# Performance work log

Hardware: AMD Instinct MI355X
Metric: run time of the kernel (lower is better)

## Reference

```python
import jax, jax.numpy as jnp
import numpy as np
from jax import lax

H = 8          # num_heads
LAM = 4.0      # lambda_scale
POOL = 8       # pool_ratio (effective, N % POOL == 0)
NS_ITERS = 5
NS_EPS = 1e-4
WHITE_EPS = 1e-5


def _lap_kernel(x, y):
    # x: [B,H,n,D], y: [B,H,m,D] -> exp(-||x_i - y_j||_1 / LAM): [B,H,n,m]
    l1 = jnp.sum(jnp.abs(x[:, :, :, None, :] - y[:, :, None, :, :]), axis=-1)
    return jnp.exp(-l1 / LAM)


def setup_inputs() -> dict:
    key = jax.random.key(0)
    ks = jax.random.split(key, 8)
    B, N, C = 2, 1024, 512
    s = 0.05  # weight scale for realistic magnitudes
    return {
        "x": jax.random.normal(ks[0], (B, N, C), jnp.float32),
        "attention_mask": jnp.ones((B, N), jnp.float32),
        "qkv_w": jax.random.normal(ks[1], (3 * C, C), jnp.float32) * s,
        "qkv_b": jax.random.normal(ks[2], (3 * C,), jnp.float32) * s,
        "proj_w": jax.random.normal(ks[3], (C, C), jnp.float32) * s,
        "proj_b": jax.random.normal(ks[4], (C,), jnp.float32) * s,
        "dwc_w": jax.random.normal(ks[5], (C, 1, 3), jnp.float32) * s,
        "dwc_b": jax.random.normal(ks[6], (C,), jnp.float32) * s,
    }


def reference(x, attention_mask, qkv_w, qkv_b, proj_w, proj_b, dwc_w, dwc_b):
    B, N, C = x.shape
    D = C // H
    tm = attention_mask                      # [B,N]
    mh = tm[:, None, :, None]                # [B,1,N,1] broadcast over heads

    qkv = (x @ qkv_w.T + qkv_b).reshape(B, N, 3, H, D).transpose(2, 0, 3, 1, 4)
    q, k, v = qkv[0] * mh, qkv[1] * mh, qkv[2] * mh   # [B,H,N,D]

    # NOTE: faithful to source: raw reshape of [B,N,H*D] into [B,C,N]
    v_sp = v.transpose(0, 2, 1, 3).reshape(B, C, N)
    q_sp = q.transpose(0, 2, 1, 3).reshape(B, C, N)
    k_sp = k.transpose(0, 2, 1, 3).reshape(B, C, N)

    # depthwise conv1d, kernel 3, padding 1
    v_local = lax.conv_general_dilated(
        v_sp, dwc_w, window_strides=(1,), padding=[(1, 1)],
        feature_group_count=C, dimension_numbers=("NCH", "OIH", "NCH")
    ) + dwc_b[None, :, None]
    v_local = v_local.transpose(0, 2, 1) * tm[:, :, None]   # [B,N,C]

    p = POOL
    m = N // p
    pm = tm.reshape(B, 1, m, p).mean(-1)                    # [B,1,m]
    pms = jnp.clip(pm, 1e-6)
    q_pool = (q_sp * tm[:, None, :]).reshape(B, C, m, p).mean(-1) / pms
    k_pool = (k_sp * tm[:, None, :]).reshape(B, C, m, p).mean(-1) / pms
    lmask = (pm > 0).astype(x.dtype)[:, 0, :]               # [B,m]

    q_l = q_pool.transpose(0, 2, 1).reshape(B, m, H, D).transpose(0, 2, 1, 3)
    k_l = k_pool.transpose(0, 2, 1).reshape(B, m, H, D).transpose(0, 2, 1, 3)

    W = _lap_kernel(q_l, k_l)                               # [B,H,m,m]
    pair = lmask[:, None, :, None] * lmask[:, None, None, :]
    I = jnp.eye(m, dtype=x.dtype)[None, None]
    W = W * pair + I * (1.0 - pair)

    # Newton-Schulz pseudo-inverse
    W_eps = W + NS_EPS * I
    fro = jnp.sqrt(jnp.sum(W_eps * W_eps, axis=(-2, -1), keepdims=True))
    X = (2.0 / (fro + 1e-8)) * jnp.swapaxes(W_eps, -2, -1)
    for _ in range(NS_ITERS):
        X = X @ (2.0 * I - W_eps @ X)
    W_inv = X

    la_mask = lmask[:, None, None, :]                        # [B,1,1,m]
    C_q = _lap_kernel(q, k_l) * la_mask                      # [B,H,N,m]
    C_k = _lap_kernel(k, q_l) * la_mask                      # [B,H,N,m]

    # batch-statistics whitening of C_q over dims (0,2)
    qmask = tm[:, None, :, None]                             # [B,1,N,1]
    valid = jnp.clip(jnp.sum(qmask, axis=(0, 2), keepdims=True), 1.0)
    mu = jnp.sum(C_q * qmask, axis=(0, 2), keepdims=True) / valid
    cen = (C_q - mu) * qmask
    var = jnp.sum(cen * cen, axis=(0, 2), keepdims=True) / valid
    C_q_norm = ((C_q - mu) / jnp.sqrt(var + WHITE_EPS)) * qmask

    context = W_inv @ (jnp.swapaxes(C_k, -2, -1) @ v)        # [B,H,m,D]
    ga = (C_q_norm @ context) * mh                           # [B,H,N,D]
    ga = ga.transpose(0, 2, 1, 3).reshape(B, N, C)

    out = (ga + v_local) @ proj_w.T + proj_b
    return out * tm[:, :, None]
```

## Files before the change

kernel.cpp:

```cpp
#include <hip/hip_runtime.h>
#include <hip/hip_bf16.h>
#include <hip/hip_fp16.h>

#define Hh 8
#define Bz 2
#define Nn 1024
#define Cc 512
#define Dd 64
#define Mm 128
#define NS_EPS 1e-4f
#define WHITE_EPS 1e-5f
#define NEG_L2E_OVER_LAM (-0.3606737602222409f)

__device__ __forceinline__ float h2f(__half v) { return __half2float(v); }
__device__ __forceinline__ __half f2h(float v) { return __float2half(v); }
__device__ __forceinline__ float lapexp(float s) {
  return __builtin_amdgcn_exp2f(s * NEG_L2E_OVER_LAM);
}

typedef _Float16 half8 __attribute__((ext_vector_type(8)));
typedef _Float16 half4v __attribute__((ext_vector_type(4)));
typedef float float4v __attribute__((ext_vector_type(4)));

__global__ __launch_bounds__(256) void qkv_gemm(
    const float* __restrict__ x, const float* __restrict__ w,
    const float* __restrict__ bias, const float* __restrict__ tm,
    __half* __restrict__ Q, __half* __restrict__ K, __half* __restrict__ V) {
  __shared__ _Float16 As[128 * 40];
  __shared__ _Float16 Bs[128 * 40];
  int m0 = blockIdx.x * 128, n0 = blockIdx.y * 128;
  int tid = threadIdx.x;
  int lane = tid & 63, wv = tid >> 6;
  int wm = (wv >> 1) * 64, wn = (wv & 1) * 64;
  int l15 = lane & 15, quad = lane >> 4;
  int srow = tid >> 1, shalf = tid & 1;
  float4v acc[4][4] = {};
  for (int k0 = 0; k0 < 512; k0 += 32) {
    __syncthreads();
    {
      const float4* ga = (const float4*)(x + (size_t)(m0 + srow) * 512 + k0 + shalf * 16);
      const float4* gb = (const float4*)(w + (size_t)(n0 + srow) * 512 + k0 + shalf * 16);
      float4 a0 = ga[0], a1 = ga[1], a2 = ga[2], a3 = ga[3];
      float4 b0 = gb[0], b1 = gb[1], b2 = gb[2], b3 = gb[3];
      half8 ha0 = {(_Float16)a0.x, (_Float16)a0.y, (_Float16)a0.z, (_Float16)a0.w,
                   (_Float16)a1.x, (_Float16)a1.y, (_Float16)a1.z, (_Float16)a1.w};
      half8 ha1 = {(_Float16)a2.x, (_Float16)a2.y, (_Float16)a2.z, (_Float16)a2.w,
                   (_Float16)a3.x, (_Float16)a3.y, (_Float16)a3.z, (_Float16)a3.w};
      half8 hb0 = {(_Float16)b0.x, (_Float16)b0.y, (_Float16)b0.z, (_Float16)b0.w,
                   (_Float16)b1.x, (_Float16)b1.y, (_Float16)b1.z, (_Float16)b1.w};
      half8 hb1 = {(_Float16)b2.x, (_Float16)b2.y, (_Float16)b2.z, (_Float16)b2.w,
                   (_Float16)b3.x, (_Float16)b3.y, (_Float16)b3.z, (_Float16)b3.w};
      int lo = srow * 40 + shalf * 16;
      *(half8*)&As[lo] = ha0;
      *(half8*)&As[lo + 8] = ha1;
      *(half8*)&Bs[lo] = hb0;
      *(half8*)&Bs[lo + 8] = hb1;
    }
    __syncthreads();
    half8 a[4], b[4];
#pragma unroll
    for (int mt = 0; mt < 4; ++mt)
      a[mt] = *(const half8*)&As[(wm + mt * 16 + l15) * 40 + quad * 8];
#pragma unroll
    for (int nt = 0; nt < 4; ++nt)
      b[nt] = *(const half8*)&Bs[(wn + nt * 16 + l15) * 40 + quad * 8];
#pragma unroll
    for (int mt = 0; mt < 4; ++mt)
#pragma unroll
      for (int nt = 0; nt < 4; ++nt)
        acc[mt][nt] =
            __builtin_amdgcn_mfma_f32_16x16x32_f16(a[mt], b[nt], acc[mt][nt], 0, 0, 0);
  }
#pragma unroll
  for (int mt = 0; mt < 4; ++mt) {
#pragma unroll
    for (int r = 0; r < 4; ++r) {
      int row = m0 + wm + mt * 16 + quad * 4 + r;
      int b_ = row >> 10, n_ = row & 1023;
      float t = tm[b_ * 1024 + n_];
#pragma unroll
      for (int nt = 0; nt < 4; ++nt) {
        int c3 = n0 + wn + nt * 16 + l15;
        float v = (acc[mt][nt][r] + bias[c3]) * t;
        int sec = c3 >> 9, ch = c3 & 511;
        __half* dst = (sec == 0) ? Q : (sec == 1 ? K : V);
        dst[(size_t)b_ * (Nn * Cc) + (size_t)n_ * 512 + ch] = f2h(v);
      }
    }
  }
}

__global__ __launch_bounds__(256) void pool_kernel(
    const __half* __restrict__ Q, const __half* __restrict__ K,
    const float* __restrict__ tm, __half* __restrict__ QL,
    __half* __restrict__ KL, float* __restrict__ LM) {
  int ut = blockIdx.x;
  int bh = blockIdx.y;
  int b = bh >> 3, h = bh & 7;
  int u0 = ut * 64;
  int delta = u0 >> 9;
  int ch0 = u0 & 511;
  __shared__ float Qs[64][65];
  __shared__ float Ks[64][65];
  int tid = threadIdx.x;
  for (int e = tid; e < 4096; e += 256) {
    int d = e >> 6, uu = e & 63;
    int row = 2 * (h * 64 + d) + delta;
    size_t gi = (size_t)b * (Nn * Cc) + (size_t)row * 512 + ch0 + uu;
    Qs[d][uu] = h2f(Q[gi]);
    Ks[d][uu] = h2f(K[gi]);
  }
  __syncthreads();
  int d = tid & 63, s = tid >> 6;
#pragma unroll
  for (int jr = 0; jr < 2; ++jr) {
    int jl = s + 4 * jr;
    int j = ut * 8 + jl;
    float pm = 0.f, sq = 0.f, sk = 0.f;
#pragma unroll
    for (int i = 0; i < 8; ++i) {
      float t = tm[b * 1024 + 8 * j + i];
      pm += t;
      sq += Qs[d][8 * jl + i] * t;
      sk += Ks[d][8 * jl + i] * t;
    }
    pm *= 0.125f;
    float pms = fmaxf(pm, 1e-6f);
    size_t oi = ((size_t)bh * 128 + j) * 64 + d;
    QL[oi] = f2h(sq * 0.125f / pms);
    KL[oi] = f2h(sk * 0.125f / pms);
    if (h == 0 && d == 0) LM[b * 128 + j] = (pm > 0.f) ? 1.f : 0.f;
  }
}

__global__ __launch_bounds__(256) void fused_phase1(
    const __half* __restrict__ Q, const __half* __restrict__ K,
    const __half* __restrict__ V, const __half* __restrict__ QL,
    const __half* __restrict__ KL, const float* __restrict__ LM,
    const float* __restrict__ tm, __half* __restrict__ Wh,
    float* __restrict__ KTVp, float* __restrict__ PS,
    __half* __restrict__ Pbuf) {
  __shared__ __align__(16) char smem[31232];
  int id = blockIdx.x;
  int tid = threadIdx.x;
  if (id < 512) {
    int jt = id & 3, bh = (id >> 2) & 15, nc = id >> 6;
    int b = bh >> 3, h = bh & 7;
    int j0 = jt * 32;
    float* kls = (float*)smem;
    float* Qs = (float*)(smem + 8704);
    float* red = (float*)(smem + 17408);
    int sr = tid >> 3, sd8 = (tid & 7) * 8;
    {
      half8 q = *(const half8*)(KL + (size_t)bh * 8192 + (size_t)(j0 + sr) * 64 + sd8);
      float4 f0 = {(float)q[0], (float)q[1], (float)q[2], (float)q[3]};
      float4 f1 = {(float)q[4], (float)q[5], (float)q[6], (float)q[7]};
      *(float4*)&kls[sr * 68 + sd8] = f0;
      *(float4*)&kls[sr * 68 + sd8 + 4] = f1;
    }
    int jq = tid & 15, nq = tid >> 4;
    int jA = j0 + jq * 2, jB = jA + 1;
    float lmA = LM[b * 128 + jA], lmB = LM[b * 128 + jB];
    float aA1 = 0.f, aA2 = 0.f, aA3 = 0.f, aB1 = 0.f, aB2 = 0.f, aB3 = 0.f;
    for (int nt = 0; nt < 4; ++nt) {
      int n0 = nc * 128 + nt * 32;
      __syncthreads();
      {
        size_t gi = (size_t)b * (Nn * Cc) + (size_t)(n0 + sr) * 512 + h * 64 + sd8;
        half8 kv = *(const half8*)(Q + gi);
        float4 k0 = {(float)kv[0], (float)kv[1], (float)kv[2], (float)kv[3]};
        float4 k1 = {(float)kv[4], (float)kv[5], (float)kv[6], (float)kv[7]};
        *(float4*)&Qs[sr * 68 + sd8] = k0;
        *(float4*)&Qs[sr * 68 + sd8 + 4] = k1;
      }
      __syncthreads();
      const float4* q0p = (const float4*)&kls[(jq * 2) * 68];
      const float4* q1p = (const float4*)&kls[(jq * 2 + 1) * 68];
      const float4* k0p = (const float4*)&Qs[(nq * 2) * 68];
      const float4* k1p = (const float4*)&Qs[(nq * 2 + 1) * 68];
      float s00 = 0.f, s01 = 0.f, s10 = 0.f, s11 = 0.f;
#pragma unroll
      for (int i = 0; i < 16; ++i) {
        int dq = (i + tid) & 15;
        float4 q0 = q0p[dq], q1 = q1p[dq];
        float4 k0 = k0p[dq], k1 = k1p[dq];
        s00 += fabsf(q0.x - k0.x) + fabsf(q0.y - k0.y) + fabsf(q0.z - k0.z) + fabsf(q0.w - k0.w);
        s01 += fabsf(q0.x - k1.x) + fabsf(q0.y - k1.y) + fabsf(q0.z - k1.z) + fabsf(q0.w - k1.w);
        s10 += fabsf(q1.x - k0.x) + fabsf(q1.y - k0.y) + fabsf(q1.z - k0.z) + fabsf(q1.w - k0.w);
        s11 += fabsf(q1.x - k1.x) + fabsf(q1.y - k1.y) + fabsf(q1.z - k1.z) + fabsf(q1.w - k1.w);
      }
      int nA = n0 + nq * 2, nB = nA + 1;
      float tA = tm[b * 1024 + nA], tB = tm[b * 1024 + nB];
      float xAa = lapexp(s00) * lmA;
      float xAb = lapexp(s01) * lmA;
      float xBa = lapexp(s10) * lmB;
      float xBb = lapexp(s11) * lmB;
      Pbuf[((size_t)bh * 1024 + nA) * 128 + jA] = f2h(xAa);
      Pbuf[((size_t)bh * 1024 + nB) * 128 + jA] = f2h(xAb);
      Pbuf[((size_t)bh * 1024 + nA) * 128 + jB] = f2h(xBa);
      Pbuf[((size_t)bh * 1024 + nB) * 128 + jB] = f2h(xBb);
      float xt;
      xt = xAa * tA; aA1 += xt; aA2 += xt * xt; aA3 += xt * tA;
      xt = xAb * tB; aA1 += xt; aA2 += xt * xt; aA3 += xt * tB;
      xt = xBa * tA; aB1 += xt; aB2 += xt * xt; aB3 += xt * tA;
      xt = xBb * tB; aB1 += xt; aB2 += xt * xt; aB3 += xt * tB;
    }
    int jl = jq * 2;
    red[(jl * 8 + nq) * 3 + 0] = aA1;
    red[(jl * 8 + nq) * 3 + 1] = aA2;
    red[(jl * 8 + nq) * 3 + 2] = aA3;
    red[((jl + 1) * 8 + nq) * 3 + 0] = aB1;
    red[((jl + 1) * 8 + nq) * 3 + 1] = aB2;
    red[((jl + 1) * 8 + nq) * 3 + 2] = aB3;
    __syncthreads();
    if (tid < 32) {
      float s1 = 0.f, s2 = 0.f, s3 = 0.f;
#pragma unroll
      for (int q = 0; q < 8; ++q) {
        s1 += red[(tid * 8 + q) * 3 + 0];
        s2 += red[(tid * 8 + q) * 3 + 1];
        s3 += red[(tid * 8 + q) * 3 + 2];
      }
      size_t base = ((size_t)(nc * 16 + bh) * 128 + j0 + tid) * 3;
      PS[base] = s1; PS[base + 1] = s2; PS[base + 2] = s3;
    }
  } else if (id < 1024) {
    int kid = id - 512;
    int jt = kid & 7, bh = (kid >> 3) & 15, nc = kid >> 7;
    int b = bh >> 3, h = bh & 7;
    int j0 = jt * 16;
    float* qls = (float*)smem;
    float* Ks = (float*)(smem + 4352);
    float* Vs = (float*)(smem + 13056);
    float* P = (float*)(smem + 21760);
    int sr = tid >> 3, sd8 = (tid & 7) * 8;
    if (tid < 128) {
      half8 q = *(const half8*)(QL + (size_t)bh * 8192 + (size_t)(j0 + sr) * 64 + sd8);
      float4 f0 = {(float)q[0], (float)q[1], (float)q[2], (float)q[3]};
      float4 f1 = {(float)q[4], (float)q[5], (float)q[6], (float)q[7]};
      *(float4*)&qls[sr * 68 + sd8] = f0;
      *(float4*)&qls[sr * 68 + sd8 + 4] = f1;
    }
    int jq = tid & 15, nq = tid >> 4;
    int jl = tid >> 4, dq4 = tid & 15;
    float acc[4] = {};
    for (int nt = 0; nt < 8; ++nt) {
      int n0 = nc * 256 + nt * 32;
      __syncthreads();
      {
        size_t gi = (size_t)b * (Nn * Cc) + (size_t)(n0 + sr) * 512 + h * 64 + sd8;
        half8 kv = *(const half8*)(K + gi);
        half8 vv = *(const half8*)(V + gi);
        float4 k0 = {(float)kv[0], (float)kv[1], (float)kv[2], (float)kv[3]};
        float4 k1 = {(float)kv[4], (float)kv[5], (float)kv[6], (float)kv[7]};
        float4 v0 = {(float)vv[0], (float)vv[1], (float)vv[2], (float)vv[3]};
        float4 v1 = {(float)vv[4], (float)vv[5], (float)vv[6], (float)vv[7]};
        *(float4*)&Ks[sr * 68 + sd8] = k0;
        *(float4*)&Ks[sr * 68 + sd8 + 4] = k1;
        *(float4*)&Vs[sr * 68 + sd8] = v0;
        *(float4*)&Vs[sr * 68 + sd8 + 4] = v1;
      }
      __syncthreads();
      {
        const float4* qp = (const float4*)&qls[jq * 68];
        const float4* k0p = (const float4*)&Ks[(nq * 2) * 68];
        const float4* k1p = (const float4*)&Ks[(nq * 2 + 1) * 68];
        float s0 = 0.f, s1 = 0.f;
#pragma unroll
        for (int i = 0; i < 16; ++i) {
          int dq = (i + tid) & 15;
          float4 qv = qp[dq];
          float4 k0 = k0p[dq], k1 = k1p[dq];
          s0 += fabsf(qv.x - k0.x) + fabsf(qv.y - k0.y) + fabsf(qv.z - k0.z) + fabsf(qv.w - k0.w);
          s1 += fabsf(qv.x - k1.x) + fabsf(qv.y - k1.y) + fabsf(qv.z - k1.z) + fabsf(qv.w - k1.w);
        }
        P[(nq * 2) * 20 + jq] = lapexp(s0);
        P[(nq * 2 + 1) * 20 + jq] = lapexp(s1);
      }
      __syncthreads();
      {
#pragma unroll 8
        for (int n = 0; n < 32; ++n) {
          float p = P[n * 20 + jl];
          float4 v = *(const float4*)&Vs[n * 68 + dq4 * 4];
          acc[0] += p * v.x; acc[1] += p * v.y; acc[2] += p * v.z; acc[3] += p * v.w;
        }
      }
    }
    {
      float lm = LM[b * 128 + j0 + jl];
      float* dst = &KTVp[((size_t)nc * 16 + bh) * 8192 + (size_t)(j0 + jl) * 64 + dq4 * 4];
      float4 o = {acc[0] * lm, acc[1] * lm, acc[2] * lm, acc[3] * lm};
      *(float4*)dst = o;
    }
  } else {
    int wid = id - 1024;
    int it = wid >> 4, bh = wid & 15;
    int b = bh >> 3;
    int i0 = it * 16;
    _Float16* kls16 = (_Float16*)smem;
    float* qs = (float*)(smem + 18432);
    float* ps = (float*)(smem + 22784);
    for (int e = tid; e < 8192; e += 256)
      kls16[(e >> 6) * 72 + (e & 63)] = (_Float16)(*(const _Float16*)&KL[(size_t)bh * 8192 + e]);
    for (int e = tid; e < 1024; e += 256)
      qs[(e >> 6) * 68 + (e & 63)] =
          h2f(QL[(size_t)bh * 8192 + (size_t)(i0 + (e >> 6)) * 64 + (e & 63)]);
    __syncthreads();
    int jg = tid & 63, ng = tid >> 6;
    int j = jg * 2;
    const _Float16* kArow = &kls16[j * 72];
    const _Float16* kBrow = &kls16[(j + 1) * 72];
    float sA[4] = {}, sB[4] = {};
#pragma unroll
    for (int i = 0; i < 16; ++i) {
      int dq = (i + jg) & 15;
      half4v k4a = *(const half4v*)&kArow[dq * 4];
      half4v k4b = *(const half4v*)&kBrow[dq * 4];
      float4 ka = {(float)k4a[0], (float)k4a[1], (float)k4a[2], (float)k4a[3]};
      float4 kb = {(float)k4b[0], (float)k4b[1], (float)k4b[2], (float)k4b[3]};
#pragma unroll
      for (int r = 0; r < 4; ++r) {
        float4 qv = *(const float4*)&qs[(ng * 4 + r) * 68 + dq * 4];
        sA[r] += fabsf(qv.x - ka.x) + fabsf(qv.y - ka.y) + fabsf(qv.z - ka.z) + fabsf(qv.w - ka.w);
        sB[r] += fabsf(qv.x - kb.x) + fabsf(qv.y - kb.y) + fabsf(qv.z - kb.z) + fabsf(qv.w - kb.w);
      }
    }
    float lmA = LM[b * Mm + j], lmB = LM[b * Mm + j + 1];
#pragma unroll
    for (int r = 0; r < 4; ++r) {
      int i = i0 + ng * 4 + r;
      float lmi = LM[b * Mm + i];
      float prA = lmi * lmA, prB = lmi * lmB;
      float dA = (i == j) ? 1.f : 0.f;
      float dB = (i == j + 1) ? 1.f : 0.f;
      ps[(ng * 4 + r) * 132 + j] = lapexp(sA[r]) * prA + dA * (1.f - prA) + dA * NS_EPS;
      ps[(ng * 4 + r) * 132 + j + 1] = lapexp(sB[r]) * prB + dB * (1.f - prB) + dB * NS_EPS;
    }
    __syncthreads();
    for (int e = tid; e < 2048; e += 256)
      Wh[(size_t)bh * (Mm * Mm) + (size_t)(i0 + (e >> 7)) * 128 + (e & 127)] =
          f2h(ps[(e >> 7) * 132 + (e & 127)]);
  }
}

__global__ __launch_bounds__(1024) void fused_phase2(
    const __half* __restrict__ Wh, const float* __restrict__ KTVp,
    const float* __restrict__ PS, const float* __restrict__ tm,
    __half* __restrict__ CTX, float* __restrict__ MU, float* __restrict__ RS) {
  __shared__ __align__(16) char smem[143360];
  int tid = threadIdx.x;
  if (blockIdx.x < 16) {
    int bh = blockIdx.x;
    _Float16* Ws = (_Float16*)smem;
    _Float16* Xa = (_Float16*)(smem + 34816);
    _Float16* Xb = (_Float16*)(smem + 69632);
    _Float16* Tt = (_Float16*)(smem + 104448);
    float* red = (float*)(smem + 139264);
    const __half* Wb = Wh + (size_t)bh * 16384;
    float fro = 0.f;
    for (int e = tid; e < 16384; e += 1024) {
      float wv = h2f(Wb[e]);
      Ws[(e >> 7) * 136 + (e & 127)] = (_Float16)wv;
      fro += wv * wv;
    }
    red[tid] = fro;
    __syncthreads();
    for (int off = 512; off > 0; off >>= 1) {
      if (tid < off) red[tid] += red[tid + off];
      __syncthreads();
    }
    float scale = 2.f / (sqrtf(red[0]) + 1e-8f);
    for (int e = tid; e < 16384; e += 1024) {
      int i = e >> 7, k = e & 127;
      Xa[i * 136 + k] = (_Float16)(scale * (float)Ws[k * 136 + i]);
      Xb[i * 136 + k] = (_Float16)(scale * (float)Ws[i * 136 + k]);
    }
    __syncthreads();
    int lane = tid & 63, wv_ = tid >> 6;
    int wm = (wv_ >> 2) * 32, wn = (wv_ & 3) * 32;
    int l15 = lane & 15, quad = lane >> 4;
    for (int it = 0; it < 5; ++it) {
      {
        float4v acc[2][2] = {};
#pragma unroll
        for (int kt = 0; kt < 4; ++kt) {
          half8 a[2], b[2];
#pragma unroll
          for (int mt = 0; mt < 2; ++mt)
            a[mt] = *(const half8*)&Ws[(wm + mt * 16 + l15) * 136 + kt * 32 + quad * 8];
#pragma unroll
          for (int nt = 0; nt < 2; ++nt)
            b[nt] = *(const half8*)&Xb[(wn + nt * 16 + l15) * 136 + kt * 32 + quad * 8];
#pragma unroll
          for (int mt = 0; mt < 2; ++mt)
#pragma unroll
            for (int nt = 0; nt < 2; ++nt)
              acc[mt][nt] =
                  __builtin_amdgcn_mfma_f32_16x16x32_f16(a[mt], b[nt], acc[mt][nt], 0, 0, 0);
        }
#pragma unroll
        for (int mt = 0; mt < 2; ++mt)
#pragma unroll
          for (int r = 0; r < 4; ++r) {
            int i = wm + mt * 16 + quad * 4 + r;
#pragma unroll
            for (int nt = 0; nt < 2; ++nt) {
              int j = wn + nt * 16 + l15;
              Tt[j * 136 + i] = (_Float16)(((i == j) ? 2.f : 0.f) - acc[mt][nt][r]);
            }
          }
      }
      __syncthreads();
      {
        float4v acc[2][2] = {};
#pragma unroll
        for (int kt = 0; kt < 4; ++kt) {
          half8 a[2], b[2];
#pragma unroll
          for (int mt = 0; mt < 2; ++mt)
            a[mt] = *(const half8*)&Xa[(wm + mt * 16 + l15) * 136 + kt * 32 + quad * 8];
#pragma unroll
          for (int nt = 0; nt < 2; ++nt)
            b[nt] = *(const half8*)&Tt[(wn + nt * 16 + l15) * 136 + kt * 32 + quad * 8];
#pragma unroll
          for (int mt = 0; mt < 2; ++mt)
#pragma unroll
            for (int nt = 0; nt < 2; ++nt)
              acc[mt][nt] =
                  __builtin_amdgcn_mfma_f32_16x16x32_f16(a[mt], b[nt], acc[mt][nt], 0, 0, 0);
        }
        __syncthreads();
#pragma unroll
        for (int mt = 0; mt < 2; ++mt)
#pragma unroll
          for (int r = 0; r < 4; ++r) {
            int i = wm + mt * 16 + quad * 4 + r;
#pragma unroll
            for (int nt = 0; nt < 2; ++nt) {
              int j = wn + nt * 16 + l15;
              _Float16 v = (_Float16)acc[mt][nt][r];
              Xa[i * 136 + j] = v;
              Xb[j * 136 + i] = v;
            }
          }
      }
      __syncthreads();
    }
    float* KTVs = (float*)smem;
    for (int e = tid; e < 8192; e += 1024) {
      float s = KTVp[(size_t)bh * 8192 + e];
#pragma unroll
      for (int nc = 1; nc < 4; ++nc) s += KTVp[((size_t)nc * 16 + bh) * 8192 + e];
      KTVs[(e >> 6) * 68 + (e & 63)] = s;
    }
    __syncthreads();
    int i = tid >> 3, d0 = (tid & 7) * 8;
    float a0 = 0.f, a1 = 0.f, a2 = 0.f, a3 = 0.f;
    float a4 = 0.f, a5 = 0.f, a6 = 0.f, a7 = 0.f;
#pragma unroll 4
    for (int j = 0; j < 128; ++j) {
      float xv = (float)Xa[i * 136 + j];
      float4 k0 = *(const float4*)&KTVs[j * 68 + d0];
      float4 k1 = *(const float4*)&KTVs[j * 68 + d0 + 4];
      a0 += xv * k0.x; a1 += xv * k0.y; a2 += xv * k0.z; a3 += xv * k0.w;
      a4 += xv * k1.x; a5 += xv * k1.y; a6 += xv * k1.z; a7 += xv * k1.w;
    }
    half8 hout = {(_Float16)a0, (_Float16)a1, (_Float16)a2, (_Float16)a3,
                  (_Float16)a4, (_Float16)a5, (_Float16)a6, (_Float16)a7};
    *(half8*)(CTX + (size_t)bh * 8192 + (size_t)i * 64 + d0) = hout;
  } else {
    float (*red2)[2] = (float(*)[2])smem;
    float* ts = (float*)(smem + 8192);
    float a = 0.f, c = 0.f;
    for (int i = tid; i < 2048; i += 1024) { float t = tm[i]; a += t; c += t * t; }
    red2[tid][0] = a; red2[tid][1] = c;
    __syncthreads();
    for (int off = 512; off > 0; off >>= 1) {
      if (tid < off) { red2[tid][0] += red2[tid + off][0]; red2[tid][1] += red2[tid + off][1]; }
      __syncthreads();
    }
    if (tid == 0) { ts[0] = red2[0][0]; ts[1] = red2[0][1]; }
    __syncthreads();
    int hj = tid;
    int h = hj >> 7, j = hj & 127;
    float s1 = 0.f, s2 = 0.f, s3 = 0.f;
#pragma unroll
    for (int nc = 0; nc < 8; ++nc)
#pragma unroll
      for (int b = 0; b < 2; ++b) {
        const float* p = PS + ((size_t)(nc * 16 + b * 8 + h) * 128 + j) * 3;
        s1 += p[0]; s2 += p[1]; s3 += p[2];
      }
    float valid = fmaxf(ts[0], 1.f);
    float mu = s1 / valid;
    float var = (s2 - 2.f * mu * s3 + mu * mu * ts[1]) / valid;
    var = fmaxf(var, 0.f);
    MU[hj] = mu;
    RS[hj] = rsqrtf(var + WHITE_EPS);
  }
}

__global__ __launch_bounds__(256) void ga_fused(
    const __half* __restrict__ Pbuf, const float* __restrict__ MU,
    const float* __restrict__ RS, const __half* __restrict__ CTXg,
    const __half* __restrict__ V, const float* __restrict__ dwc_w,
    const float* __restrict__ dwc_b, const float* __restrict__ tm,
    __half* __restrict__ VL) {
  int bh = blockIdx.y;
  int b = bh >> 3, h = bh & 7;
  int n0 = blockIdx.x * 32;
  __shared__ __half Ps[32][130];
  __shared__ __align__(16) __half2 ctx2[128][32];
  __shared__ float musr[128][2];
  int tid = threadIdx.x;
  for (int e = tid; e < 4096; e += 256)
    Ps[e >> 7][e & 127] = Pbuf[((size_t)bh * 1024 + n0 + (e >> 7)) * 128 + (e & 127)];
  {
    const __half2* cg = (const __half2*)(CTXg + (size_t)bh * 8192);
    for (int e = tid; e < 4096; e += 256) ctx2[e >> 5][e & 31] = cg[e];
  }
  if (tid < 128) { musr[tid][0] = MU[h * 128 + tid]; musr[tid][1] = RS[h * 128 + tid]; }
  __syncthreads();
  int nn = tid >> 4, dq = tid & 15;
  float acc[2][4] = {};
#pragma unroll 2
  for (int j = 0; j < 128; ++j) {
    float mu = musr[j][0], rs = musr[j][1];
    uint2 cc = *(const uint2*)&ctx2[j][dq * 2];
    __half2 c01 = __builtin_bit_cast(__half2, cc.x);
    __half2 c23 = __builtin_bit_cast(__half2, cc.y);
    float c0 = h2f(c01.x), c1 = h2f(c01.y), c2 = h2f(c23.x), c3 = h2f(c23.y);
#pragma unroll
    for (int rr = 0; rr < 2; ++rr) {
      float pj = (h2f(Ps[nn + rr * 16][j]) - mu) * rs;
      acc[rr][0] += pj * c0; acc[rr][1] += pj * c1;
      acc[rr][2] += pj * c2; acc[rr][3] += pj * c3;
    }
  }
#pragma unroll
  for (int rr = 0; rr < 2; ++rr) {
    int t = n0 + nn + rr * 16;
    float tmv = tm[b * 1024 + t];
    float t2 = tmv * tmv;
    float o[4] = {acc[rr][0] * t2, acc[rr][1] * t2, acc[rr][2] * t2, acc[rr][3] * t2};
#pragma unroll
    for (int q = 0; q < 4; ++q) {
      int c = h * 64 + dq * 4 + q;
      float vacc = dwc_b[c];
#pragma unroll
      for (int k = 0; k < 3; ++k) {
        int u = t - 1 + k;
        if (u >= 0 && u < 1024) {
          int n = 2 * c + (u >> 9), ch = u & 511;
          vacc += dwc_w[c * 3 + k] * h2f(V[(size_t)b * (Nn * Cc) + (size_t)n * 512 + ch]);
        }
      }
      o[q] += vacc * tmv;
    }
    size_t base = (size_t)b * (Nn * Cc) + (size_t)t * 512 + h * 64 + dq * 4;
    VL[base] = f2h(o[0]);
    VL[base + 1] = f2h(o[1]);
    VL[base + 2] = f2h(o[2]);
    VL[base + 3] = f2h(o[3]);
  }
}

__global__ __launch_bounds__(256) void proj_gemm(
    const __half* __restrict__ Ain, const float* __restrict__ w,
    const float* __restrict__ bias, const float* __restrict__ tm,
    float* __restrict__ out) {
  __shared__ _Float16 As[64 * 40];
  __shared__ _Float16 Bs[64 * 40];
  int m0 = blockIdx.x * 64, n0 = blockIdx.y * 64;
  int tid = threadIdx.x;
  int lane = tid & 63, wv = tid >> 6;
  int wm = (wv >> 1) * 32, wn = (wv & 1) * 32;
  int l15 = lane & 15, quad = lane >> 4;
  int srow = tid >> 2, scol = (tid & 3) * 8;
  float4v acc[2][2] = {};
  for (int k0 = 0; k0 < 512; k0 += 32) {
    __syncthreads();
    {
      half8 ha = *(const half8*)(Ain + (size_t)(m0 + srow) * 512 + k0 + scol);
      const float4* gb = (const float4*)(w + (size_t)(n0 + srow) * 512 + k0 + scol);
      float4 b0 = gb[0], b1 = gb[1];
      half8 hb = {(_Float16)b0.x, (_Float16)b0.y, (_Float16)b0.z, (_Float16)b0.w,
                  (_Float16)b1.x, (_Float16)b1.y, (_Float16)b1.z, (_Float16)b1.w};
      int lo = srow * 40 + scol;
      *(half8*)&As[lo] = ha;
      *(half8*)&Bs[lo] = hb;
    }
    __syncthreads();
    half8 a[2], b[2];
#pragma unroll
    for (int mt = 0; mt < 2; ++mt)
      a[mt] = *(const half8*)&As[(wm + mt * 16 + l15) * 40 + quad * 8];
#pragma unroll
    for (int nt = 0; nt < 2; ++nt)
      b[nt] = *(const half8*)&Bs[(wn + nt * 16 + l15) * 40 + quad * 8];
#pragma unroll
    for (int mt = 0; mt < 2; ++mt)
#pragma unroll
      for (int nt = 0; nt < 2; ++nt)
        acc[mt][nt] =
            __builtin_amdgcn_mfma_f32_16x16x32_f16(a[mt], b[nt], acc[mt][nt], 0, 0, 0);
  }
#pragma unroll
  for (int mt = 0; mt < 2; ++mt) {
#pragma unroll
    for (int r = 0; r < 4; ++r) {
      int row = m0 + wm + mt * 16 + quad * 4 + r;
      int b_ = row >> 10, n_ = row & 1023;
      float t = tm[b_ * 1024 + n_];
#pragma unroll
      for (int nt = 0; nt < 2; ++nt) {
        int co = n0 + wn + nt * 16 + l15;
        out[(size_t)row * 512 + co] = (acc[mt][nt][r] + bias[co]) * t;
      }
    }
  }
}

extern "C" void kernel_launch(void* const* d_in, const int* in_sizes, int n_in,
                              void* d_out, int out_size, void* d_ws, size_t ws_size,
                              hipStream_t stream) {
  const float* x      = (const float*)d_in[0];
  const float* tm     = (const float*)d_in[1];
  const float* qkv_w  = (const float*)d_in[2];
  const float* qkv_b  = (const float*)d_in[3];
  const float* proj_w = (const float*)d_in[4];
  const float* proj_b = (const float*)d_in[5];
  const float* dwc_w  = (const float*)d_in[6];
  const float* dwc_b  = (const float*)d_in[7];
  float* out = (float*)d_out;

  char* wsb = (char*)d_ws;
  __half* Qh  = (__half*)(wsb + 0);
  __half* Kh  = (__half*)(wsb + 2097152);
  __half* Vh  = (__half*)(wsb + 4194304);
  __half* VLh = (__half*)(wsb + 6291456);
  float*  KTVp = (float*)(wsb + 6291456);
  __half* QLh = (__half*)(wsb + 8388608);
  __half* KLh = (__half*)(wsb + 8650752);
  float*  LM  = (float*)(wsb + 8912896);
  float*  MU  = (float*)(wsb + 8913920);
  float*  RS  = (float*)(wsb + 8918016);
  __half* CTX = (__half*)(wsb + 8922112);
  float*  PS  = (float*)(wsb + 9184256);
  __half* Wh  = (__half*)(wsb + 9380864);

  __half* Pbuf = (__half*)d_out;

  qkv_gemm<<<dim3(16, 12), 256, 0, stream>>>(x, qkv_w, qkv_b, tm, Qh, Kh, Vh);
  pool_kernel<<<dim3(16, 16), 256, 0, stream>>>(Qh, Kh, tm, QLh, KLh, LM);
  fused_phase1<<<1152, 256, 0, stream>>>(Qh, Kh, Vh, QLh, KLh, LM, tm, Wh, KTVp,
                                         PS, Pbuf);
  fused_phase2<<<17, 1024, 0, stream>>>(Wh, KTVp, PS, tm, CTX, MU, RS);
  ga_fused<<<dim3(32, 16), 256, 0, stream>>>(Pbuf, MU, RS, CTX, Vh, dwc_w, dwc_b, tm, VLh);
  proj_gemm<<<dim3(32, 8), 256, 0, stream>>>(VLh, proj_w, proj_b, tm, out);
}
```

Baseline: 201.3 us.

## Fuse pooling into phase1 blocks and drop separate pool kernel

Removes the standalone pool_kernel launch and computes the pooled Q/K landmarks and landmark mask inside each fused_phase1 block, straight from the Q/K buffers. This saves a launch and the global round trip for QL/KL/LM. In exchange every block redoes its share of the pooling, and the W blocks each pool all 128 K landmarks, which adds redundant loads and arithmetic. The W staging buffer also moves from fp32 to fp16 in shared memory.

```diff
diff --git a/kernel.cpp b/kernel.cpp
--- a/kernel.cpp
+++ b/kernel.cpp
@@ -90,56 +90,11 @@
   }
 }
 
-__global__ __launch_bounds__(256) void pool_kernel(
-    const __half* __restrict__ Q, const __half* __restrict__ K,
-    const float* __restrict__ tm, __half* __restrict__ QL,
-    __half* __restrict__ KL, float* __restrict__ LM) {
-  int ut = blockIdx.x;
-  int bh = blockIdx.y;
-  int b = bh >> 3, h = bh & 7;
-  int u0 = ut * 64;
-  int delta = u0 >> 9;
-  int ch0 = u0 & 511;
-  __shared__ float Qs[64][65];
-  __shared__ float Ks[64][65];
-  int tid = threadIdx.x;
-  for (int e = tid; e < 4096; e += 256) {
-    int d = e >> 6, uu = e & 63;
-    int row = 2 * (h * 64 + d) + delta;
-    size_t gi = (size_t)b * (Nn * Cc) + (size_t)row * 512 + ch0 + uu;
-    Qs[d][uu] = h2f(Q[gi]);
-    Ks[d][uu] = h2f(K[gi]);
-  }
-  __syncthreads();
-  int d = tid & 63, s = tid >> 6;
-#pragma unroll
-  for (int jr = 0; jr < 2; ++jr) {
-    int jl = s + 4 * jr;
-    int j = ut * 8 + jl;
-    float pm = 0.f, sq = 0.f, sk = 0.f;
-#pragma unroll
-    for (int i = 0; i < 8; ++i) {
-      float t = tm[b * 1024 + 8 * j + i];
-      pm += t;
-      sq += Qs[d][8 * jl + i] * t;
-      sk += Ks[d][8 * jl + i] * t;
-    }
-    pm *= 0.125f;
-    float pms = fmaxf(pm, 1e-6f);
-    size_t oi = ((size_t)bh * 128 + j) * 64 + d;
-    QL[oi] = f2h(sq * 0.125f / pms);
-    KL[oi] = f2h(sk * 0.125f / pms);
-    if (h == 0 && d == 0) LM[b * 128 + j] = (pm > 0.f) ? 1.f : 0.f;
-  }
-}
-
 __global__ __launch_bounds__(256) void fused_phase1(
     const __half* __restrict__ Q, const __half* __restrict__ K,
-    const __half* __restrict__ V, const __half* __restrict__ QL,
-    const __half* __restrict__ KL, const float* __restrict__ LM,
-    const float* __restrict__ tm, __half* __restrict__ Wh,
-    float* __restrict__ KTVp, float* __restrict__ PS,
-    __half* __restrict__ Pbuf) {
+    const __half* __restrict__ V, const float* __restrict__ tm,
+    __half* __restrict__ Wh, float* __restrict__ KTVp,
+    float* __restrict__ PS, __half* __restrict__ Pbuf) {
   __shared__ __align__(16) char smem[31232];
   int id = blockIdx.x;
   int tid = threadIdx.x;
@@ -148,23 +103,45 @@
     int b = bh >> 3, h = bh & 7;
     int j0 = jt * 32;
     float* kls = (float*)smem;
-    float* Qs = (float*)(smem + 8704);
+    float* Qs  = (float*)(smem + 8704);
     float* red = (float*)(smem + 17408);
+    float* tms = (float*)(smem + 20480);
+    float* pmi = (float*)(smem + 21504);
+    float* lmv = (float*)(smem + 21632);
+    int u0 = j0 * 8;
+    tms[tid] = tm[b * 1024 + u0 + tid];
+    __syncthreads();
+    if (tid < 32) {
+      float pm = 0.f;
+#pragma unroll
+      for (int i = 0; i < 8; ++i) pm += tms[tid * 8 + i];
+      pm *= 0.125f;
+      pmi[tid] = 0.125f / fmaxf(pm, 1e-6f);
+      lmv[tid] = (pm > 0.f) ? 1.f : 0.f;
+    }
+    __syncthreads();
+    {
+      const __half* Kb = K + (size_t)b * (Nn * Cc) + (size_t)(h * 64) * 1024;
+#pragma unroll
+      for (int k = 0; k < 8; ++k) {
+        int g = k * 256 + tid;
+        int c = g >> 5, jl = g & 31;
+        half8 v = *(const half8*)(Kb + (size_t)c * 1024 + u0 + jl * 8);
+        float s = 0.f;
+#pragma unroll
+        for (int i = 0; i < 8; ++i) s += (float)v[i] * tms[jl * 8 + i];
+        kls[jl * 68 + c] = s * pmi[jl];
+      }
+    }
     int sr = tid >> 3, sd8 = (tid & 7) * 8;
-    {
-      half8 q = *(const half8*)(KL + (size_t)bh * 8192 + (size_t)(j0 + sr) * 64 + sd8);
-      float4 f0 = {(float)q[0], (float)q[1], (float)q[2], (float)q[3]};
-      float4 f1 = {(float)q[4], (float)q[5], (float)q[6], (float)q[7]};
-      *(float4*)&kls[sr * 68 + sd8] = f0;
-      *(float4*)&kls[sr * 68 + sd8 + 4] = f1;
-    }
     int jq = tid & 15, nq = tid >> 4;
+    float lmA = 0.f, lmB = 0.f;
+    float aA1 = 0.f, aA2 = 0.f, aA3 = 0.f, aB1 = 0.f, aB2 = 0.f, aB3 = 0.f;
     int jA = j0 + jq * 2, jB = jA + 1;
-    float lmA = LM[b * 128 + jA], lmB = LM[b * 128 + jB];
-    float aA1 = 0.f, aA2 = 0.f, aA3 = 0.f, aB1 = 0.f, aB2 = 0.f, aB3 = 0.f;
     for (int nt = 0; nt < 4; ++nt) {
       int n0 = nc * 128 + nt * 32;
       __syncthreads();
+      if (nt == 0) { lmA = lmv[jq * 2]; lmB = lmv[jq * 2 + 1]; }
       {
         size_t gi = (size_t)b * (Nn * Cc) + (size_t)(n0 + sr) * 512 + h * 64 + sd8;
         half8 kv = *(const half8*)(Q + gi);
@@ -230,17 +207,38 @@
     int b = bh >> 3, h = bh & 7;
     int j0 = jt * 16;
     float* qls = (float*)smem;
-    float* Ks = (float*)(smem + 4352);
-    float* Vs = (float*)(smem + 13056);
-    float* P = (float*)(smem + 21760);
+    float* Ks  = (float*)(smem + 4352);
+    float* Vs  = (float*)(smem + 13056);
+    float* P   = (float*)(smem + 21760);
+    float* tms = (float*)(smem + 24320);
+    float* pmi = (float*)(smem + 24832);
+    float* lmv = (float*)(smem + 24896);
+    int u0 = j0 * 8;
+    if (tid < 128) tms[tid] = tm[b * 1024 + u0 + tid];
+    __syncthreads();
+    if (tid < 16) {
+      float pm = 0.f;
+#pragma unroll
+      for (int i = 0; i < 8; ++i) pm += tms[tid * 8 + i];
+      pm *= 0.125f;
+      pmi[tid] = 0.125f / fmaxf(pm, 1e-6f);
+      lmv[tid] = (pm > 0.f) ? 1.f : 0.f;
+    }
+    __syncthreads();
+    {
+      const __half* Qb = Q + (size_t)b * (Nn * Cc) + (size_t)(h * 64) * 1024;
+#pragma unroll
+      for (int k = 0; k < 4; ++k) {
+        int g = k * 256 + tid;
+        int c = g >> 4, jl = g & 15;
+        half8 v = *(const half8*)(Qb + (size_t)c * 1024 + u0 + jl * 8);
+        float s = 0.f;
+#pragma unroll
+        for (int i = 0; i < 8; ++i) s += (float)v[i] * tms[jl * 8 + i];
+        qls[jl * 68 + c] = s * pmi[jl];
+      }
+    }
     int sr = tid >> 3, sd8 = (tid & 7) * 8;
-    if (tid < 128) {
-      half8 q = *(const half8*)(QL + (size_t)bh * 8192 + (size_t)(j0 + sr) * 64 + sd8);
-      float4 f0 = {(float)q[0], (float)q[1], (float)q[2], (float)q[3]};
-      float4 f1 = {(float)q[4], (float)q[5], (float)q[6], (float)q[7]};
-      *(float4*)&qls[sr * 68 + sd8] = f0;
-      *(float4*)&qls[sr * 68 + sd8 + 4] = f1;
-    }
     int jq = tid & 15, nq = tid >> 4;
     int jl = tid >> 4, dq4 = tid & 15;
     float acc[4] = {};
@@ -288,7 +286,7 @@
       }
     }
     {
-      float lm = LM[b * 128 + j0 + jl];
+      float lm = lmv[jl];
       float* dst = &KTVp[((size_t)nc * 16 + bh) * 8192 + (size_t)(j0 + jl) * 64 + dq4 * 4];
       float4 o = {acc[0] * lm, acc[1] * lm, acc[2] * lm, acc[3] * lm};
       *(float4*)dst = o;
@@ -296,16 +294,48 @@
   } else {
     int wid = id - 1024;
     int it = wid >> 4, bh = wid & 15;
-    int b = bh >> 3;
+    int b = bh >> 3, h = bh & 7;
     int i0 = it * 16;
     _Float16* kls16 = (_Float16*)smem;
-    float* qs = (float*)(smem + 18432);
-    float* ps = (float*)(smem + 22784);
-    for (int e = tid; e < 8192; e += 256)
-      kls16[(e >> 6) * 72 + (e & 63)] = (_Float16)(*(const _Float16*)&KL[(size_t)bh * 8192 + e]);
-    for (int e = tid; e < 1024; e += 256)
-      qs[(e >> 6) * 68 + (e & 63)] =
-          h2f(QL[(size_t)bh * 8192 + (size_t)(i0 + (e >> 6)) * 64 + (e & 63)]);
+    float* qs  = (float*)(smem + 18432);
+    float* pm2 = (float*)(smem + 22784);
+    float* tms = (float*)(smem + 23808);
+    _Float16* ps16 = (_Float16*)(smem + 23808);
+    for (int e = tid; e < 1024; e += 256) tms[e] = tm[b * 1024 + e];
+    __syncthreads();
+    if (tid < 128) {
+      float pm = 0.f;
+#pragma unroll
+      for (int i = 0; i < 8; ++i) pm += tms[tid * 8 + i];
+      pm *= 0.125f;
+      pm2[tid * 2] = 0.125f / fmaxf(pm, 1e-6f);
+      pm2[tid * 2 + 1] = (pm > 0.f) ? 1.f : 0.f;
+    }
+    __syncthreads();
+    {
+      const __half* Kb = K + (size_t)b * (Nn * Cc) + (size_t)(h * 64) * 1024;
+      const __half* Qb = Q + (size_t)b * (Nn * Cc) + (size_t)(h * 64) * 1024;
+#pragma unroll
+      for (int k = 0; k < 32; ++k) {
+        int g = k * 256 + tid;
+        int c = g >> 7, j = g & 127;
+        half8 v = *(const half8*)(Kb + (size_t)c * 1024 + j * 8);
+        float s = 0.f;
+#pragma unroll
+        for (int i = 0; i < 8; ++i) s += (float)v[i] * tms[j * 8 + i];
+        kls16[j * 72 + c] = (_Float16)(s * pm2[j * 2]);
+      }
+#pragma unroll
+      for (int k = 0; k < 4; ++k) {
+        int g = k * 256 + tid;
+        int c = g >> 4, il = g & 15;
+        half8 v = *(const half8*)(Qb + (size_t)c * 1024 + (i0 + il) * 8);
+        float s = 0.f;
+#pragma unroll
+        for (int i = 0; i < 8; ++i) s += (float)v[i] * tms[(i0 + il) * 8 + i];
+        qs[il * 68 + c] = s * pm2[(i0 + il) * 2];
+      }
+    }
     __syncthreads();
     int jg = tid & 63, ng = tid >> 6;
     int j = jg * 2;
@@ -326,21 +356,25 @@
         sB[r] += fabsf(qv.x - kb.x) + fabsf(qv.y - kb.y) + fabsf(qv.z - kb.z) + fabsf(qv.w - kb.w);
       }
     }
-    float lmA = LM[b * Mm + j], lmB = LM[b * Mm + j + 1];
+    float lmA = pm2[j * 2 + 1], lmB = pm2[(j + 1) * 2 + 1];
 #pragma unroll
     for (int r = 0; r < 4; ++r) {
       int i = i0 + ng * 4 + r;
-      float lmi = LM[b * Mm + i];
+      float lmi = pm2[i * 2 + 1];
       float prA = lmi * lmA, prB = lmi * lmB;
       float dA = (i == j) ? 1.f : 0.f;
       float dB = (i == j + 1) ? 1.f : 0.f;
-      ps[(ng * 4 + r) * 132 + j] = lapexp(sA[r]) * prA + dA * (1.f - prA) + dA * NS_EPS;
-      ps[(ng * 4 + r) * 132 + j + 1] = lapexp(sB[r]) * prB + dB * (1.f - prB) + dB * NS_EPS;
-    }
-    __syncthreads();
-    for (int e = tid; e < 2048; e += 256)
+      ps16[(ng * 4 + r) * 132 + j] =
+          (_Float16)(lapexp(sA[r]) * prA + dA * (1.f - prA) + dA * NS_EPS);
+      ps16[(ng * 4 + r) * 132 + j + 1] =
+          (_Float16)(lapexp(sB[r]) * prB + dB * (1.f - prB) + dB * NS_EPS);
+    }
+    __syncthreads();
+    for (int e = tid; e < 2048; e += 256) {
+      _Float16 v = ps16[(e >> 7) * 132 + (e & 127)];
       Wh[(size_t)bh * (Mm * Mm) + (size_t)(i0 + (e >> 7)) * 128 + (e & 127)] =
-          f2h(ps[(e >> 7) * 132 + (e & 127)]);
+          *(__half*)&v;
+    }
   }
 }
 
@@ -641,9 +675,6 @@
   __half* Vh  = (__half*)(wsb + 4194304);
   __half* VLh = (__half*)(wsb + 6291456);
   float*  KTVp = (float*)(wsb + 6291456);
-  __half* QLh = (__half*)(wsb + 8388608);
-  __half* KLh = (__half*)(wsb + 8650752);
-  float*  LM  = (float*)(wsb + 8912896);
   float*  MU  = (float*)(wsb + 8913920);
   float*  RS  = (float*)(wsb + 8918016);
   __half* CTX = (__half*)(wsb + 8922112);
@@ -653,9 +684,7 @@
   __half* Pbuf = (__half*)d_out;
 
   qkv_gemm<<<dim3(16, 12), 256, 0, stream>>>(x, qkv_w, qkv_b, tm, Qh, Kh, Vh);
-  pool_kernel<<<dim3(16, 16), 256, 0, stream>>>(Qh, Kh, tm, QLh, KLh, LM);
-  fused_phase1<<<1152, 256, 0, stream>>>(Qh, Kh, Vh, QLh, KLh, LM, tm, Wh, KTVp,
-                                         PS, Pbuf);
+  fused_phase1<<<1152, 256, 0, stream>>>(Qh, Kh, Vh, tm, Wh, KTVp, PS, Pbuf);
   fused_phase2<<<17, 1024, 0, stream>>>(Wh, KTVp, PS, tm, CTX, MU, RS);
   ga_fused<<<dim3(32, 16), 256, 0, stream>>>(Pbuf, MU, RS, CTX, Vh, dwc_w, dwc_b, tm, VLh);
   proj_gemm<<<dim3(32, 8), 256, 0, stream>>>(VLh, proj_w, proj_b, tm, out);
```

Measured after the change: 200.4 us. Within noise of the previous version (-0.5%).
